# Optimization experiments

Measured on AMD Instinct MI355X. Metric: run time of the kernel, lower is better.

Reference implementation:

```python
import jax, jax.numpy as jnp
import numpy as np
import math

N_NODES = 50000
M = 200000          # number of (node, hyperedge) incidences
NE = 20000          # number of hyperedges (= hyperedge_index[1].max()+1)
NI = 8              # num_inds (inducing points)
DIN = 64            # dim_in
DV = 64             # dim_out == dim_V
NH = 4              # num_heads
DH = DV // NH


def setup_inputs() -> dict:
    key = jax.random.key(0)
    ks = jax.random.split(key, 24)
    node_idx = jax.random.randint(ks[0], (M,), 0, N_NODES, dtype=jnp.int32)
    edge_idx = jax.random.randint(ks[1], (M,), 0, NE, dtype=jnp.int32)
    # guarantee num_edges == NE (matches num_edges = max+1 in torch code)
    edge_idx = edge_idx.at[-1].set(NE - 1)
    hyperedge_index = jnp.stack([node_idx, edge_idx], axis=0)

    def lin(k, fan_in, shape):
        return jax.random.normal(k, shape, dtype=jnp.float32) / np.sqrt(fan_in)

    inp = {
        "X": jax.random.normal(ks[2], (N_NODES, DIN), dtype=jnp.float32),
        "hyperedge_index": hyperedge_index,
        "I": lin(ks[3], DV, (NI, DV)),  # xavier-ish inducing points
    }
    names = ["m0_wq", "m0_bq", "m0_wk", "m0_bk", "m0_wv", "m0_bv", "m0_wo", "m0_bo",
             "m1_wq", "m1_bq", "m1_wk", "m1_bk", "m1_wv", "m1_bv", "m1_wo", "m1_bo"]
    for i, n in enumerate(names):
        k = ks[4 + i]
        if n.endswith("b" + n[-1]) and n[3] == 'b':
            inp[n] = lin(k, DV, (DV,))
        else:
            inp[n] = lin(k, DV, (DV, DV))
    return inp


def _segment_softmax(a, seg, num_segments):
    # a: [E, NH]; segment-wise stable softmax along E grouped by seg
    amax = jax.ops.segment_max(a, seg, num_segments=num_segments)
    amax = jnp.where(jnp.isfinite(amax), amax, jnp.zeros_like(amax))
    e = jnp.exp(a - amax[seg])
    den = jax.ops.segment_sum(e, seg, num_segments=num_segments)
    return e / den[seg]


def _mab(Qin, Kin, wq, bq, wk, bk, wv, bv, wo, bo,
         q_idx, k_idx, seg, out_idx, num_segments):
    Q = Qin @ wq + bq            # [Nq, DV]
    K = Kin @ wk + bk            # [Nk, DV]
    V = Kin @ wv + bv            # [Nk, DV]
    # gather per extended edge, split into heads: [E, NH, DH]
    Qi = Q[q_idx].reshape(-1, NH, DH)
    Kj = K[k_idx].reshape(-1, NH, DH)
    Vj = V[k_idx].reshape(-1, NH, DH)
    A = (Qi * Kj).sum(-1) / math.sqrt(DV)               # [E, NH]
    A = _segment_softmax(A, seg, num_segments)           # segment softmax over LE_index
    QKV = jax.ops.segment_sum(A[..., None] * Vj, seg, num_segments=num_segments)  # [ns, NH, DH]
    O = Q[out_idx].reshape(-1, NH, DH) + QKV              # [ns, NH, DH]
    # torch: stack heads at dim0 then permute(1,2,0).reshape -> [N, DH, NH] flatten
    O = jnp.transpose(O, (0, 2, 1)).reshape(-1, DV)
    return O + jax.nn.relu(O @ wo + bo)


def reference(X, hyperedge_index, I,
              m0_wq, m0_bq, m0_wk, m0_bk, m0_wv, m0_bv, m0_wo, m0_bo,
              m1_wq, m1_bq, m1_wk, m1_bk, m1_wv, m1_bv, m1_wo, m1_bo):
    node = hyperedge_index[0]                 # [M]
    edge = hyperedge_index[1]                 # [M]
    node_t = jnp.tile(node, NI)               # [M*NI]
    edge_t = jnp.tile(edge, NI)
    inc = jnp.repeat(jnp.arange(NI, dtype=edge.dtype), M)
    ext2 = edge_t * NI + inc                  # index into I_big rows / segments for mab0

    I_big = jnp.tile(I, (NE, 1))              # [NE*NI, DV]
    # mab0: queries = inducing points (per edge), keys/values = X
    H = _mab(I_big, X,
             m0_wq, m0_bq, m0_wk, m0_bk, m0_wv, m0_bv, m0_wo, m0_bo,
             q_idx=ext2, k_idx=node_t, seg=ext2,
             out_idx=jnp.arange(NE * NI), num_segments=NE * NI)

    seg1 = jnp.tile(jnp.arange(M, dtype=edge.dtype), NI)
    # mab1: queries = X, keys/values = H; output one row per incidence
    O = _mab(X, H,
             m1_wq, m1_bq, m1_wk, m1_bk, m1_wv, m1_bv, m1_wo, m1_bo,
             q_idx=node_t, k_idx=ext2, seg=seg1,
             out_idx=node, num_segments=M)
    return O  # [M, DV]; original returns (O, None)
```

## Files before the change

kernel.cpp:

```cpp
#include <hip/hip_runtime.h>
#include <math.h>

#define NNODES 50000
#define MINC   200000
#define NEDGE  20000
#define NIND   8

#define SCALE_LOG2E 0.18033688f

typedef __attribute__((ext_vector_type(8))) short bf16x8;
typedef __attribute__((ext_vector_type(4))) float f32x4;

__device__ __forceinline__ short f2bf(float f) {
    union { float f; unsigned u; } x; x.f = f;
    unsigned r = x.u + 0x7FFF + ((x.u >> 16) & 1);
    return (short)(r >> 16);
}
__device__ __forceinline__ float bf2f(short s) {
    union { unsigned u; float f; } x; x.u = ((unsigned)(unsigned short)s) << 16;
    return x.f;
}
__device__ __forceinline__ int qperm(int c) { return ((c & 15) << 2) | (c >> 4); }
__device__ __forceinline__ int sigperm(int c) { return ((c & 3) << 4) | (c >> 2); }

__global__ void setup_hist_kernel(const float* __restrict__ I,
                                  const float* __restrict__ m0_wq, const float* __restrict__ m0_bq,
                                  const float* __restrict__ m0_wk, const float* __restrict__ m0_bk,
                                  const float* __restrict__ m0_wv, const float* __restrict__ m0_bv,
                                  const float* __restrict__ m1_wq, const float* __restrict__ m1_bq,
                                  const float* __restrict__ m0_wo, const float* __restrict__ m1_wk,
                                  const float* __restrict__ m1_wv, const float* __restrict__ m1_wo,
                                  float* __restrict__ QI, float* __restrict__ bias160,
                                  short* __restrict__ Wt0, short* __restrict__ WtO,
                                  short* __restrict__ WtK, short* __restrict__ WtV,
                                  short* __restrict__ WtF,
                                  const int* __restrict__ edge, int* __restrict__ cnt) {
    __shared__ float QIs[512];
    __shared__ float Wf[2048];
    __shared__ float bfS[32];
    int tid = threadIdx.x, bid = blockIdx.x;
    if (bid >= 6) {
        int m = (bid - 6) * 512 + tid;
        if (m < MINC) atomicAdd(&cnt[edge[m]], 1);
        return;
    }
    {
        int i = tid >> 6, c = tid & 63;
        float acc = m0_bq[c];
        for (int k = 0; k < 64; ++k) acc += I[i * 64 + k] * m0_wq[k * 64 + c];
        QIs[tid] = acc;
    }
    __syncthreads();
    if (bid == 0) {
        QI[tid] = QIs[tid];
        if (tid < 32) {
            int i = tid >> 2, h = tid & 3;
            float s = 0.f;
            for (int d = 0; d < 16; ++d)
                s += m0_bk[h * 16 + d] * QIs[i * 64 + h * 16 + d];
            bfS[tid] = s * SCALE_LOG2E;
        }
        __syncthreads();
        if (tid < 160)
            bias160[tid] = (tid < 64) ? m0_bv[tid]
                         : ((tid < 96) ? bfS[tid - 64] : m1_bq[tid - 96]);
    } else if (bid == 1) {
        for (int idx = tid; idx < 2048; idx += 512) {
            int k = idx >> 5, j = idx & 31;
            int i = j >> 2, h = j & 3;
            float s = 0.f;
            for (int d = 0; d < 16; ++d)
                s += m0_wk[k * 64 + h * 16 + d] * QIs[i * 64 + h * 16 + d];
            Wf[idx] = s * SCALE_LOG2E;
        }
        __syncthreads();
        for (int idx = tid; idx < 160 * 72; idx += 512) {
            int c = idx / 72, k = idx % 72;
            short v = 0;
            if (k < 64) {
                float f = (c < 64) ? m0_wv[k * 64 + c]
                        : (c < 96) ? Wf[k * 32 + (c - 64)]
                                   : m1_wq[k * 64 + (c - 96)];
                v = f2bf(f);
            }
            Wt0[idx] = v;
        }
    } else {
        int mat = bid - 2;
        const float* W = (mat == 0) ? m0_wo : (mat == 1) ? m1_wk : (mat == 2) ? m1_wv : m1_wo;
        short* D = (mat == 0) ? WtO : (mat == 1) ? WtK : (mat == 2) ? WtV : WtF;
        bool cperm = (mat == 0);
        for (int idx = tid; idx < 64 * 72; idx += 512) {
            int c = idx / 72, k = idx % 72;
            short v = 0;
            if (k < 64) {
                int kk = qperm(k);
                int cc = cperm ? qperm(c) : c;
                v = f2bf(W[kk * 64 + cc]);
            }
            D[idx] = v;
        }
    }
}

#define NALLOCB ((NEDGE + 255) / 256)
__global__ void gemmx_alloc_kernel(const float* __restrict__ A,
                                   const short* __restrict__ Wt, const float* __restrict__ bias,
                                   short* __restrict__ V0, _Float16* __restrict__ S0,
                                   short* __restrict__ Q1,
                                   const int* __restrict__ cnt, int2* __restrict__ rowcnt,
                                   int* __restrict__ cursor, int* __restrict__ total) {
    __shared__ short As[64 * 72];
    __shared__ short Ws[160 * 72];
    int tid = threadIdx.x;
    if (blockIdx.x < NALLOCB) {
        int e = blockIdx.x * 256 + tid;
        int lane = tid & 63;
        int c = (e < NEDGE) ? cnt[e] : 0;
        int v = c;
        #pragma unroll
        for (int off = 1; off < 64; off <<= 1) {
            int t = __shfl_up(v, off);
            if (lane >= off) v += t;
        }
        int wavesum = __shfl(v, 63);
        int base = 0;
        if (lane == 63) base = atomicAdd(total, wavesum);
        base = __shfl(base, 63);
        int excl = base + v - c;
        if (e < NEDGE) {
            rowcnt[e] = make_int2(excl, c);
            cursor[e] = excl;
        }
        return;
    }
    int row0 = (blockIdx.x - NALLOCB) * 64;
    {
        const uint4* wsrc = (const uint4*)Wt;
        uint4* wdst = (uint4*)Ws;
        for (int k = tid; k < 1440; k += 256) wdst[k] = wsrc[k];
    }
    {
        int r = tid >> 2, c0 = (tid & 3) * 16;
        int gr = row0 + r;
        float f[16];
        if (gr < NNODES) {
            const float4* src = (const float4*)(A + (size_t)gr * 64 + c0);
            #pragma unroll
            for (int j = 0; j < 4; ++j) {
                float4 t4 = src[j];
                f[4*j] = t4.x; f[4*j+1] = t4.y; f[4*j+2] = t4.z; f[4*j+3] = t4.w;
            }
        } else {
            #pragma unroll
            for (int j = 0; j < 16; ++j) f[j] = 0.f;
        }
        short tmp[16];
        #pragma unroll
        for (int j = 0; j < 16; ++j) tmp[j] = f2bf(f[j]);
        uint4* dst = (uint4*)&As[r * 72 + c0];
        dst[0] = *(const uint4*)&tmp[0];
        dst[1] = *(const uint4*)&tmp[8];
    }
    __syncthreads();
    int w = tid >> 6, l = tid & 63;
    int lr16 = l & 15, lk = (l >> 4) * 8;
    f32x4 acc[10] = {};
    #pragma unroll
    for (int ks = 0; ks < 2; ++ks) {
        bf16x8 a = *(const bf16x8*)&As[(w * 16 + lr16) * 72 + ks * 32 + lk];
        #pragma unroll
        for (int t = 0; t < 10; ++t) {
            bf16x8 b = *(const bf16x8*)&Ws[(t * 16 + lr16) * 72 + ks * 32 + lk];
            acc[t] = __builtin_amdgcn_mfma_f32_16x16x32_bf16(a, b, acc[t], 0, 0, 0);
        }
    }
    int rbase = w * 16 + (l >> 4) * 4;
    #pragma unroll
    for (int t = 0; t < 10; ++t) {
        int c = t * 16 + lr16;
        float bb = bias[c];
        #pragma unroll
        for (int r = 0; r < 4; ++r) {
            int gr = row0 + rbase + r;
            if (gr < NNODES) {
                float val = acc[t][r] + bb;
                if (c < 64) V0[(size_t)gr * 64 + c] = f2bf(val);
                else if (c < 96) S0[(size_t)gr * 32 + (c - 64)] = (_Float16)val;
                else Q1[(size_t)gr * 64 + (c - 96)] = f2bf(val);
            }
        }
    }
}

__global__ void scatter_kernel(const int* __restrict__ node, const int* __restrict__ edge,
                               int* __restrict__ cursor, int2* __restrict__ csr_nm) {
    int m = blockIdx.x * 256 + threadIdx.x;
    if (m < MINC) {
        int e = edge[m];
        int pos = atomicAdd(&cursor[e], 1);
        csr_nm[pos] = make_int2(node[m], m);
    }
}

#define CH0 32
__global__ void attn0_kernel(const short* __restrict__ V0, const _Float16* __restrict__ S0,
                             const float* __restrict__ QI,
                             const int2* __restrict__ rowcnt, const int2* __restrict__ csr_nm,
                             short* __restrict__ Opre0) {
    __shared__ float Sw[4][CH0][32];
    __shared__ float Sc[4][32];
    __shared__ float Li[4][32];
    __shared__ int   Ns[4][CH0];
    int w = threadIdx.x >> 6;
    int lane = threadIdx.x & 63;
    int e = blockIdx.x * 4 + w;
    int2 rc = rowcnt[e];
    int start = rc.x, end = rc.x + rc.y;
    int j = lane & 31;
    int pslot = lane >> 5;
    int tj = ((j & 3) << 3) | (j >> 2);
    int col2 = lane & 31;
    int hh = col2 >> 3;
    float runm = -INFINITY, lrun = 0.f;
    float accL[8] = {}, accH[8] = {};
    for (int c0 = start; c0 < end; c0 += CH0) {
        int cnt = min(CH0, end - c0);
        if (lane < CH0) {
            int idx = c0 + min(lane, cnt - 1);
            Ns[w][lane] = csr_nm[idx].x;
        }
        asm volatile("s_waitcnt lgkmcnt(0)" ::: "memory");
        __builtin_amdgcn_sched_barrier(0);
        float cm = -INFINITY;
        for (int p = pslot; p < cnt; p += 2) {
            int n = Ns[w][p];
            float s = (float)S0[(size_t)n * 32 + j];
            Sw[w][p][tj] = s;
            cm = fmaxf(cm, s);
        }
        cm = fmaxf(cm, __shfl_xor(cm, 32));
        float newm = fmaxf(runm, cm);
        float sc = exp2f(runm - newm);
        runm = newm;
        float lsum = 0.f;
        for (int p = pslot; p < cnt; p += 2) {
            float s = Sw[w][p][tj];
            float w_ = exp2f(s - newm);
            Sw[w][p][tj] = w_;
            lsum += w_;
        }
        lsum += __shfl_xor(lsum, 32);
        lrun = lrun * sc + lsum;
        if (pslot == 0) Sc[w][tj] = sc;
        asm volatile("s_waitcnt lgkmcnt(0)" ::: "memory");
        __builtin_amdgcn_sched_barrier(0);
        float4 sA = *(const float4*)&Sc[w][hh * 8];
        float4 sB = *(const float4*)&Sc[w][hh * 8 + 4];
        accL[0] *= sA.x; accH[0] *= sA.x;
        accL[1] *= sA.y; accH[1] *= sA.y;
        accL[2] *= sA.z; accH[2] *= sA.z;
        accL[3] *= sA.w; accH[3] *= sA.w;
        accL[4] *= sB.x; accH[4] *= sB.x;
        accL[5] *= sB.y; accH[5] *= sB.y;
        accL[6] *= sB.z; accH[6] *= sB.z;
        accL[7] *= sB.w; accH[7] *= sB.w;
        int npair = (cnt + 1) >> 1;
        #pragma unroll 4
        for (int k = 0; k < npair; ++k) {
            int rp = 2 * k + pslot;
            bool vld = rp < cnt;
            int rc2 = vld ? rp : (cnt - 1);
            int n = Ns[w][rc2];
            unsigned vp = *(const unsigned*)&V0[(size_t)n * 64 + col2 * 2];
            float vlo = vld ? __int_as_float(vp << 16) : 0.f;
            float vhi = vld ? __int_as_float(vp & 0xffff0000u) : 0.f;
            float4 wA = *(const float4*)&Sw[w][rc2][hh * 8];
            float4 wB = *(const float4*)&Sw[w][rc2][hh * 8 + 4];
            accL[0] += wA.x * vlo; accH[0] += wA.x * vhi;
            accL[1] += wA.y * vlo; accH[1] += wA.y * vhi;
            accL[2] += wA.z * vlo; accH[2] += wA.z * vhi;
            accL[3] += wA.w * vlo; accH[3] += wA.w * vhi;
            accL[4] += wB.x * vlo; accH[4] += wB.x * vhi;
            accL[5] += wB.y * vlo; accH[5] += wB.y * vhi;
            accL[6] += wB.z * vlo; accH[6] += wB.z * vhi;
            accL[7] += wB.w * vlo; accH[7] += wB.w * vhi;
        }
    }
    if (pslot == 0) Li[w][tj] = lrun;
    asm volatile("s_waitcnt lgkmcnt(0)" ::: "memory");
    __builtin_amdgcn_sched_barrier(0);
    #pragma unroll
    for (int i = 0; i < 8; ++i) {
        accL[i] += __shfl_xor(accL[i], 32);
        accH[i] += __shfl_xor(accH[i], 32);
    }
    float4 lA = *(const float4*)&Li[w][hh * 8];
    float4 lB = *(const float4*)&Li[w][hh * 8 + 4];
    float li[8] = {lA.x, lA.y, lA.z, lA.w, lB.x, lB.y, lB.z, lB.w};
    if (pslot == 0) {
        #pragma unroll
        for (int i = 0; i < 8; ++i) {
            float2 qi2 = *(const float2*)&QI[i * 64 + col2 * 2];
            float inv = (li[i] > 0.f) ? 1.f / li[i] : 0.f;
            float ol = qi2.x + accL[i] * inv;
            float oh = qi2.y + accH[i] * inv;
            unsigned res = ((unsigned)(unsigned short)f2bf(oh) << 16)
                         | (unsigned)(unsigned short)f2bf(ol);
            *(unsigned*)&Opre0[(size_t)(e * NIND + i) * 64 + col2 * 2] = res;
        }
    }
}

__global__ void fused_hkv_attn1_kernel(const short* __restrict__ Opre0,
                                       const short* __restrict__ WtO, const float* __restrict__ bo,
                                       const short* __restrict__ WtK, const float* __restrict__ bk,
                                       const short* __restrict__ WtV, const float* __restrict__ bv,
                                       const short* __restrict__ Q1,
                                       const int2* __restrict__ rowcnt,
                                       const int2* __restrict__ csr_nm,
                                       short* __restrict__ Opre1) {
    __shared__ short As[64 * 72];
    __shared__ short Vls[64 * 72];
    int tid = threadIdx.x;
    int row0 = blockIdx.x * 64;
    {
        int r = tid >> 2, c0 = (tid & 3) * 16;
        const uint4* src = (const uint4*)(Opre0 + (size_t)(row0 + r) * 64 + c0);
        uint4* dst = (uint4*)&As[r * 72 + c0];
        dst[0] = src[0]; dst[1] = src[1];
    }
    __syncthreads();
    int w = tid >> 6, lane = tid & 63;
    int lr16 = lane & 15, lk = (lane >> 4) * 8;
    int rbase = w * 16 + (lane >> 4) * 4;
    {
        f32x4 acc[4] = {};
        #pragma unroll
        for (int ks = 0; ks < 2; ++ks) {
            bf16x8 a = *(const bf16x8*)&As[(w * 16 + lr16) * 72 + ks * 32 + lk];
            #pragma unroll
            for (int t = 0; t < 4; ++t) {
                bf16x8 b = *(const bf16x8*)&WtO[(t * 16 + lr16) * 72 + ks * 32 + lk];
                acc[t] = __builtin_amdgcn_mfma_f32_16x16x32_bf16(a, b, acc[t], 0, 0, 0);
            }
        }
        #pragma unroll
        for (int t = 0; t < 4; ++t) {
            int c = t * 16 + lr16;
            float bb = bo[qperm(c)];
            #pragma unroll
            for (int r = 0; r < 4; ++r) {
                float res = bf2f(As[(rbase + r) * 72 + c]);
                float hv = res + fmaxf(acc[t][r] + bb, 0.f);
                As[(rbase + r) * 72 + c] = f2bf(hv);
            }
        }
    }
    {
        f32x4 ak[4] = {}, av[4] = {};
        #pragma unroll
        for (int ks = 0; ks < 2; ++ks) {
            bf16x8 a = *(const bf16x8*)&As[(w * 16 + lr16) * 72 + ks * 32 + lk];
            #pragma unroll
            for (int t = 0; t < 4; ++t) {
                bf16x8 b1 = *(const bf16x8*)&WtK[(t * 16 + lr16) * 72 + ks * 32 + lk];
                ak[t] = __builtin_amdgcn_mfma_f32_16x16x32_bf16(a, b1, ak[t], 0, 0, 0);
                bf16x8 b2 = *(const bf16x8*)&WtV[(t * 16 + lr16) * 72 + ks * 32 + lk];
                av[t] = __builtin_amdgcn_mfma_f32_16x16x32_bf16(a, b2, av[t], 0, 0, 0);
            }
        }
        #pragma unroll
        for (int t = 0; t < 4; ++t) {
            int c = t * 16 + lr16;
            float bbk = bk[c], bbv = bv[c];
            #pragma unroll
            for (int r = 0; r < 4; ++r) {
                int rr = rbase + r;
                As[rr * 72 + c]  = f2bf((ak[t][r] + bbk) * SCALE_LOG2E);
                Vls[rr * 72 + c] = f2bf(av[t][r] + bbv);
            }
        }
    }
    int sl4 = lane & 15;
    int inc = lane >> 4;
    for (int le = 0; le < 2; ++le) {
        int eloc = w * 2 + le;
        int e = blockIdx.x * 8 + eloc;
        int lr0 = eloc * 8;
        float Kf[8][4], Vf[8][4];
        #pragma unroll
        for (int i = 0; i < 8; ++i) {
            uint2 kp = *(const uint2*)&As[(lr0 + i) * 72 + sl4 * 4];
            uint2 vp = *(const uint2*)&Vls[(lr0 + i) * 72 + sl4 * 4];
            Kf[i][0] = __int_as_float(kp.x << 16);
            Kf[i][1] = __int_as_float(kp.x & 0xffff0000u);
            Kf[i][2] = __int_as_float(kp.y << 16);
            Kf[i][3] = __int_as_float(kp.y & 0xffff0000u);
            Vf[i][0] = __int_as_float(vp.x << 16);
            Vf[i][1] = __int_as_float(vp.x & 0xffff0000u);
            Vf[i][2] = __int_as_float(vp.y << 16);
            Vf[i][3] = __int_as_float(vp.y & 0xffff0000u);
        }
        #pragma unroll
        for (int i = 0; i < 8; ++i) {
            #pragma unroll
            for (int d = 0; d < 4; ++d) {
                asm volatile("" : "+v"(Kf[i][d]), "+v"(Vf[i][d]));
            }
        }
        int2 rc = rowcnt[e];
        int start = rc.x, end = rc.x + rc.y;
        #pragma unroll 4
        for (int p0 = start; p0 < end; p0 += 4) {
            int p = p0 + inc;
            bool valid = (p < end);
            int pc = valid ? p : (end - 1);
            int2 nm = csr_nm[pc];
            uint2 qp = *(const uint2*)&Q1[(size_t)nm.x * 64 + sl4 * 4];
            float qa0 = __int_as_float(qp.x << 16);
            float qa1 = __int_as_float(qp.x & 0xffff0000u);
            float qa2 = __int_as_float(qp.y << 16);
            float qa3 = __int_as_float(qp.y & 0xffff0000u);
            float a[8];
            #pragma unroll
            for (int i = 0; i < 8; ++i) {
                float t = qa0 * Kf[i][0] + qa1 * Kf[i][1] + qa2 * Kf[i][2] + qa3 * Kf[i][3];
                int tv = __builtin_amdgcn_update_dpp(0, __float_as_int(t), 0xB1, 0xf, 0xf, true);
                t += __int_as_float(tv);
                tv = __builtin_amdgcn_update_dpp(0, __float_as_int(t), 0x4E, 0xf, 0xf, true);
                t += __int_as_float(tv);
                a[i] = t;
            }
            float mx = fmaxf(fmaxf(fmaxf(a[0], a[1]), fmaxf(a[2], a[3])),
                             fmaxf(fmaxf(a[4], a[5]), fmaxf(a[6], a[7])));
            float l = 0.f, ac0 = 0.f, ac1 = 0.f, ac2 = 0.f, ac3 = 0.f;
            #pragma unroll
            for (int i = 0; i < 8; ++i) {
                float w_ = exp2f(a[i] - mx);
                l += w_;
                ac0 += w_ * Vf[i][0];
                ac1 += w_ * Vf[i][1];
                ac2 += w_ * Vf[i][2];
                ac3 += w_ * Vf[i][3];
            }
            float rl = 1.f / l;
            float o0 = qa0 + ac0 * rl;
            float o1 = qa1 + ac1 * rl;
            float o2 = qa2 + ac2 * rl;
            float o3 = qa3 + ac3 * rl;
            uint2 res;
            res.x = ((unsigned)(unsigned short)f2bf(o1) << 16) | (unsigned)(unsigned short)f2bf(o0);
            res.y = ((unsigned)(unsigned short)f2bf(o3) << 16) | (unsigned)(unsigned short)f2bf(o2);
            if (valid) *(uint2*)&Opre1[(size_t)nm.y * 64 + sl4 * 4] = res;
        }
    }
}

__global__ void gemm_out_kernel(const short* __restrict__ Av,
                                const short* __restrict__ Wt, const float* __restrict__ bias,
                                float* __restrict__ out) {
    __shared__ short As[128 * 72];
    __shared__ short Ws[64 * 72];
    int tid = threadIdx.x;
    int row0 = blockIdx.x * 128;
    {
        const uint4* wsrc = (const uint4*)Wt;
        uint4* wdst = (uint4*)Ws;
        for (int k = tid; k < 576; k += 256) wdst[k] = wsrc[k];
    }
    #pragma unroll
    for (int it = 0; it < 2; ++it) {
        int slot = tid + it * 256;
        int r = slot >> 2, c0 = (slot & 3) * 16;
        int gr = row0 + r;
        uint4 a0 = {}, a1 = {};
        if (gr < MINC) {
            const uint4* src = (const uint4*)(Av + (size_t)gr * 64 + c0);
            a0 = src[0]; a1 = src[1];
        }
        uint4* dst = (uint4*)&As[r * 72 + c0];
        dst[0] = a0; dst[1] = a1;
    }
    __syncthreads();
    int w = tid >> 6, l = tid & 63;
    int lr16 = l & 15, lk = (l >> 4) * 8;
    f32x4 acc[2][4] = {};
    #pragma unroll
    for (int ks = 0; ks < 2; ++ks) {
        bf16x8 a0 = *(const bf16x8*)&As[(w * 16 + lr16) * 72 + ks * 32 + lk];
        bf16x8 a1 = *(const bf16x8*)&As[(64 + w * 16 + lr16) * 72 + ks * 32 + lk];
        #pragma unroll
        for (int t = 0; t < 4; ++t) {
            bf16x8 b = *(const bf16x8*)&Ws[(t * 16 + lr16) * 72 + ks * 32 + lk];
            acc[0][t] = __builtin_amdgcn_mfma_f32_16x16x32_bf16(a0, b, acc[0][t], 0, 0, 0);
            acc[1][t] = __builtin_amdgcn_mfma_f32_16x16x32_bf16(a1, b, acc[1][t], 0, 0, 0);
        }
    }
    int rbase = w * 16 + (l >> 4) * 4;
    #pragma unroll
    for (int rt = 0; rt < 2; ++rt) {
        #pragma unroll
        for (int t = 0; t < 4; ++t) {
            int c = t * 16 + lr16;
            float bb = bias[c];
            int sc = sigperm(c);
            #pragma unroll
            for (int r = 0; r < 4; ++r) {
                int gr = row0 + rt * 64 + rbase + r;
                if (gr < MINC) {
                    float val = acc[rt][t][r] + bb;
                    float res = bf2f(As[(rt * 64 + rbase + r) * 72 + sc]);
                    __builtin_nontemporal_store(res + fmaxf(val, 0.f),
                                                &out[(size_t)gr * 64 + c]);
                }
            }
        }
    }
}

extern "C" void kernel_launch(void* const* d_in, const int* in_sizes, int n_in,
                              void* d_out, int out_size, void* d_ws, size_t ws_size,
                              hipStream_t stream) {
    const float* X    = (const float*)d_in[0];
    const int*   hei  = (const int*)d_in[1];
    const float* I    = (const float*)d_in[2];
    const float* m0_wq = (const float*)d_in[3];
    const float* m0_bq = (const float*)d_in[4];
    const float* m0_wk = (const float*)d_in[5];
    const float* m0_bk = (const float*)d_in[6];
    const float* m0_wv = (const float*)d_in[7];
    const float* m0_bv = (const float*)d_in[8];
    const float* m0_wo = (const float*)d_in[9];
    const float* m0_bo = (const float*)d_in[10];
    const float* m1_wq = (const float*)d_in[11];
    const float* m1_bq = (const float*)d_in[12];
    const float* m1_wk = (const float*)d_in[13];
    const float* m1_bk = (const float*)d_in[14];
    const float* m1_wv = (const float*)d_in[15];
    const float* m1_bv = (const float*)d_in[16];
    const float* m1_wo = (const float*)d_in[17];
    const float* m1_bo = (const float*)d_in[18];

    const int* node = hei;
    const int* edge = hei + MINC;
    float* out = (float*)d_out;

    char* B = (char*)d_ws;
    short* Opre0 = (short*)B;
    short* V0    = (short*)(B + 20480000);
    _Float16* S0 = (_Float16*)(B + 26880000);
    short* Opre1 = (short*)(B + 33280000);
    short* Q1    = (short*)(B + 74240000);
    float* QI    = (float*)(B + 80640000);
    float* bias160 = QI + 512;
    short* PK    = (short*)(bias160 + 160);
    short* Wt0   = PK;
    short* WtO   = PK + 11520;
    short* WtK   = WtO + 4608;
    short* WtV   = WtK + 4608;
    short* WtF   = WtV + 4608;
    int*   ib       = (int*)(((size_t)(WtF + 4608) + 7) & ~(size_t)7);
    int2*  rowcnt   = (int2*)ib;
    int*   cnt      = (int*)(rowcnt + NEDGE);
    int*   total    = cnt + NEDGE;
    int*   cursor   = total + 1;
    int2*  csr_nm   = (int2*)(((size_t)(cursor + NEDGE) + 7) & ~(size_t)7);

    hipMemsetAsync(cnt, 0, (NEDGE + 1) * sizeof(int), stream);
    setup_hist_kernel<<<6 + (MINC + 511) / 512, 512, 0, stream>>>(
        I, m0_wq, m0_bq, m0_wk, m0_bk, m0_wv, m0_bv,
        m1_wq, m1_bq, m0_wo, m1_wk, m1_wv, m1_wo,
        QI, bias160, Wt0, WtO, WtK, WtV, WtF, edge, cnt);
    gemmx_alloc_kernel<<<NALLOCB + (NNODES + 63) / 64, 256, 0, stream>>>(
        X, Wt0, bias160, V0, S0, Q1, cnt, rowcnt, cursor, total);
    scatter_kernel<<<(MINC + 255) / 256, 256, 0, stream>>>(node, edge, cursor, csr_nm);

    attn0_kernel<<<NEDGE / 4, 256, 0, stream>>>(V0, S0, QI, rowcnt, csr_nm, Opre0);

    fused_hkv_attn1_kernel<<<NEDGE / 8, 256, 0, stream>>>(
        Opre0, WtO, m0_bo, WtK, m1_bk, WtV, m1_bv, Q1, rowcnt, csr_nm, Opre1);
    gemm_out_kernel<<<(MINC + 127) / 128, 256, 0, stream>>>(Opre1, WtF, m1_bo, out);
}
```

Baseline: 146.9 us.

## Fuse first-MAB attention into the H/K/V + second attention kernel

The separate attn0 kernel is merged into the fused H-projection/attn1 kernel. Each wave now computes the inducing-point attention for two hyperedges and writes the bf16 result straight into its own LDS rows, instead of round-tripping the Opre0 buffer through global memory. This removes one kernel launch and the global write and re-read of that intermediate, and compacts the workspace layout. In exchange, each wave processes its two edges serially, the grid has half as many waves for the attention phase, and per-block LDS grows, which may lower occupancy.

After: 149.0 us. Within noise of the previous version (+1.4%).

```diff
diff --git a/kernel.cpp b/kernel.cpp
--- a/kernel.cpp
+++ b/kernel.cpp
@@ -204,134 +204,125 @@
 }
 
 #define CH0 32
-__global__ void attn0_kernel(const short* __restrict__ V0, const _Float16* __restrict__ S0,
-                             const float* __restrict__ QI,
-                             const int2* __restrict__ rowcnt, const int2* __restrict__ csr_nm,
-                             short* __restrict__ Opre0) {
+__global__ void mega_mab1_kernel(const short* __restrict__ V0, const _Float16* __restrict__ S0,
+                                 const float* __restrict__ QI,
+                                 const short* __restrict__ WtO, const float* __restrict__ bo,
+                                 const short* __restrict__ WtK, const float* __restrict__ bk,
+                                 const short* __restrict__ WtV, const float* __restrict__ bv,
+                                 const short* __restrict__ Q1,
+                                 const int2* __restrict__ rowcnt,
+                                 const int2* __restrict__ csr_nm,
+                                 short* __restrict__ Opre1) {
+    __shared__ short As[64 * 72];
+    __shared__ short Vls[64 * 72];
     __shared__ float Sw[4][CH0][32];
     __shared__ float Sc[4][32];
     __shared__ float Li[4][32];
     __shared__ int   Ns[4][CH0];
-    int w = threadIdx.x >> 6;
-    int lane = threadIdx.x & 63;
-    int e = blockIdx.x * 4 + w;
-    int2 rc = rowcnt[e];
-    int start = rc.x, end = rc.x + rc.y;
+    int tid = threadIdx.x;
+    int w = tid >> 6, lane = tid & 63;
+
     int j = lane & 31;
     int pslot = lane >> 5;
     int tj = ((j & 3) << 3) | (j >> 2);
     int col2 = lane & 31;
     int hh = col2 >> 3;
-    float runm = -INFINITY, lrun = 0.f;
-    float accL[8] = {}, accH[8] = {};
-    for (int c0 = start; c0 < end; c0 += CH0) {
-        int cnt = min(CH0, end - c0);
-        if (lane < CH0) {
-            int idx = c0 + min(lane, cnt - 1);
-            Ns[w][lane] = csr_nm[idx].x;
-        }
+    for (int le = 0; le < 2; ++le) {
+        int e = blockIdx.x * 8 + w * 2 + le;
+        int2 rc = rowcnt[e];
+        int start = rc.x, end = rc.x + rc.y;
+        float runm = -INFINITY, lrun = 0.f;
+        float accL[8] = {}, accH[8] = {};
+        for (int c0 = start; c0 < end; c0 += CH0) {
+            int cnt = min(CH0, end - c0);
+            if (lane < CH0) {
+                int idx = c0 + min(lane, cnt - 1);
+                Ns[w][lane] = csr_nm[idx].x;
+            }
+            asm volatile("s_waitcnt lgkmcnt(0)" ::: "memory");
+            __builtin_amdgcn_sched_barrier(0);
+            float cm = -INFINITY;
+            for (int p = pslot; p < cnt; p += 2) {
+                int n = Ns[w][p];
+                float s = (float)S0[(size_t)n * 32 + j];
+                Sw[w][p][tj] = s;
+                cm = fmaxf(cm, s);
+            }
+            cm = fmaxf(cm, __shfl_xor(cm, 32));
+            float newm = fmaxf(runm, cm);
+            float sc = exp2f(runm - newm);
+            runm = newm;
+            float lsum = 0.f;
+            for (int p = pslot; p < cnt; p += 2) {
+                float s = Sw[w][p][tj];
+                float w_ = exp2f(s - newm);
+                Sw[w][p][tj] = w_;
+                lsum += w_;
+            }
+            lsum += __shfl_xor(lsum, 32);
+            lrun = lrun * sc + lsum;
+            if (pslot == 0) Sc[w][tj] = sc;
+            asm volatile("s_waitcnt lgkmcnt(0)" ::: "memory");
+            __builtin_amdgcn_sched_barrier(0);
+            float4 sA = *(const float4*)&Sc[w][hh * 8];
+            float4 sB = *(const float4*)&Sc[w][hh * 8 + 4];
+            accL[0] *= sA.x; accH[0] *= sA.x;
+            accL[1] *= sA.y; accH[1] *= sA.y;
+            accL[2] *= sA.z; accH[2] *= sA.z;
+            accL[3] *= sA.w; accH[3] *= sA.w;
+            accL[4] *= sB.x; accH[4] *= sB.x;
+            accL[5] *= sB.y; accH[5] *= sB.y;
+            accL[6] *= sB.z; accH[6] *= sB.z;
+            accL[7] *= sB.w; accH[7] *= sB.w;
+            int npair = (cnt + 1) >> 1;
+            #pragma unroll 4
+            for (int k = 0; k < npair; ++k) {
+                int rp = 2 * k + pslot;
+                bool vld = rp < cnt;
+                int rc2 = vld ? rp : (cnt - 1);
+                int n = Ns[w][rc2];
+                unsigned vp = *(const unsigned*)&V0[(size_t)n * 64 + col2 * 2];
+                float vlo = vld ? __int_as_float(vp << 16) : 0.f;
+                float vhi = vld ? __int_as_float(vp & 0xffff0000u) : 0.f;
+                float4 wA = *(const float4*)&Sw[w][rc2][hh * 8];
+                float4 wB = *(const float4*)&Sw[w][rc2][hh * 8 + 4];
+                accL[0] += wA.x * vlo; accH[0] += wA.x * vhi;
+                accL[1] += wA.y * vlo; accH[1] += wA.y * vhi;
+                accL[2] += wA.z * vlo; accH[2] += wA.z * vhi;
+                accL[3] += wA.w * vlo; accH[3] += wA.w * vhi;
+                accL[4] += wB.x * vlo; accH[4] += wB.x * vhi;
+                accL[5] += wB.y * vlo; accH[5] += wB.y * vhi;
+                accL[6] += wB.z * vlo; accH[6] += wB.z * vhi;
+                accL[7] += wB.w * vlo; accH[7] += wB.w * vhi;
+            }
+        }
+        if (pslot == 0) Li[w][tj] = lrun;
         asm volatile("s_waitcnt lgkmcnt(0)" ::: "memory");
         __builtin_amdgcn_sched_barrier(0);
-        float cm = -INFINITY;
-        for (int p = pslot; p < cnt; p += 2) {
-            int n = Ns[w][p];
-            float s = (float)S0[(size_t)n * 32 + j];
-            Sw[w][p][tj] = s;
-            cm = fmaxf(cm, s);
-        }
-        cm = fmaxf(cm, __shfl_xor(cm, 32));
-        float newm = fmaxf(runm, cm);
-        float sc = exp2f(runm - newm);
-        runm = newm;
-        float lsum = 0.f;
-        for (int p = pslot; p < cnt; p += 2) {
-            float s = Sw[w][p][tj];
-            float w_ = exp2f(s - newm);
-            Sw[w][p][tj] = w_;
-            lsum += w_;
-        }
-        lsum += __shfl_xor(lsum, 32);
-        lrun = lrun * sc + lsum;
-        if (pslot == 0) Sc[w][tj] = sc;
-        asm volatile("s_waitcnt lgkmcnt(0)" ::: "memory");
-        __builtin_amdgcn_sched_barrier(0);
-        float4 sA = *(const float4*)&Sc[w][hh * 8];
-        float4 sB = *(const float4*)&Sc[w][hh * 8 + 4];
-        accL[0] *= sA.x; accH[0] *= sA.x;
-        accL[1] *= sA.y; accH[1] *= sA.y;
-        accL[2] *= sA.z; accH[2] *= sA.z;
-        accL[3] *= sA.w; accH[3] *= sA.w;
-        accL[4] *= sB.x; accH[4] *= sB.x;
-        accL[5] *= sB.y; accH[5] *= sB.y;
-        accL[6] *= sB.z; accH[6] *= sB.z;
-        accL[7] *= sB.w; accH[7] *= sB.w;
-        int npair = (cnt + 1) >> 1;
-        #pragma unroll 4
-        for (int k = 0; k < npair; ++k) {
-            int rp = 2 * k + pslot;
-            bool vld = rp < cnt;
-            int rc2 = vld ? rp : (cnt - 1);
-            int n = Ns[w][rc2];
-            unsigned vp = *(const unsigned*)&V0[(size_t)n * 64 + col2 * 2];
-            float vlo = vld ? __int_as_float(vp << 16) : 0.f;
-            float vhi = vld ? __int_as_float(vp & 0xffff0000u) : 0.f;
-            float4 wA = *(const float4*)&Sw[w][rc2][hh * 8];
-            float4 wB = *(const float4*)&Sw[w][rc2][hh * 8 + 4];
-            accL[0] += wA.x * vlo; accH[0] += wA.x * vhi;
-            accL[1] += wA.y * vlo; accH[1] += wA.y * vhi;
-            accL[2] += wA.z * vlo; accH[2] += wA.z * vhi;
-            accL[3] += wA.w * vlo; accH[3] += wA.w * vhi;
-            accL[4] += wB.x * vlo; accH[4] += wB.x * vhi;
-            accL[5] += wB.y * vlo; accH[5] += wB.y * vhi;
-            accL[6] += wB.z * vlo; accH[6] += wB.z * vhi;
-            accL[7] += wB.w * vlo; accH[7] += wB.w * vhi;
-        }
-    }
-    if (pslot == 0) Li[w][tj] = lrun;
+        #pragma unroll
+        for (int i = 0; i < 8; ++i) {
+            accL[i] += __shfl_xor(accL[i], 32);
+            accH[i] += __shfl_xor(accH[i], 32);
+        }
+        float4 lA = *(const float4*)&Li[w][hh * 8];
+        float4 lB = *(const float4*)&Li[w][hh * 8 + 4];
+        float li[8] = {lA.x, lA.y, lA.z, lA.w, lB.x, lB.y, lB.z, lB.w};
+        if (pslot == 0) {
+            #pragma unroll
+            for (int i = 0; i < 8; ++i) {
+                float2 qi2 = *(const float2*)&QI[i * 64 + col2 * 2];
+                float inv = (li[i] > 0.f) ? 1.f / li[i] : 0.f;
+                float ol = qi2.x + accL[i] * inv;
+                float oh = qi2.y + accH[i] * inv;
+                unsigned res = ((unsigned)(unsigned short)f2bf(oh) << 16)
+                             | (unsigned)(unsigned short)f2bf(ol);
+                *(unsigned*)&As[(w * 16 + le * 8 + i) * 72 + col2 * 2] = res;
+            }
+        }
+    }
     asm volatile("s_waitcnt lgkmcnt(0)" ::: "memory");
     __builtin_amdgcn_sched_barrier(0);
-    #pragma unroll
-    for (int i = 0; i < 8; ++i) {
-        accL[i] += __shfl_xor(accL[i], 32);
-        accH[i] += __shfl_xor(accH[i], 32);
-    }
-    float4 lA = *(const float4*)&Li[w][hh * 8];
-    float4 lB = *(const float4*)&Li[w][hh * 8 + 4];
-    float li[8] = {lA.x, lA.y, lA.z, lA.w, lB.x, lB.y, lB.z, lB.w};
-    if (pslot == 0) {
-        #pragma unroll
-        for (int i = 0; i < 8; ++i) {
-            float2 qi2 = *(const float2*)&QI[i * 64 + col2 * 2];
-            float inv = (li[i] > 0.f) ? 1.f / li[i] : 0.f;
-            float ol = qi2.x + accL[i] * inv;
-            float oh = qi2.y + accH[i] * inv;
-            unsigned res = ((unsigned)(unsigned short)f2bf(oh) << 16)
-                         | (unsigned)(unsigned short)f2bf(ol);
-            *(unsigned*)&Opre0[(size_t)(e * NIND + i) * 64 + col2 * 2] = res;
-        }
-    }
-}
-
-__global__ void fused_hkv_attn1_kernel(const short* __restrict__ Opre0,
-                                       const short* __restrict__ WtO, const float* __restrict__ bo,
-                                       const short* __restrict__ WtK, const float* __restrict__ bk,
-                                       const short* __restrict__ WtV, const float* __restrict__ bv,
-                                       const short* __restrict__ Q1,
-                                       const int2* __restrict__ rowcnt,
-                                       const int2* __restrict__ csr_nm,
-                                       short* __restrict__ Opre1) {
-    __shared__ short As[64 * 72];
-    __shared__ short Vls[64 * 72];
-    int tid = threadIdx.x;
-    int row0 = blockIdx.x * 64;
-    {
-        int r = tid >> 2, c0 = (tid & 3) * 16;
-        const uint4* src = (const uint4*)(Opre0 + (size_t)(row0 + r) * 64 + c0);
-        uint4* dst = (uint4*)&As[r * 72 + c0];
-        dst[0] = src[0]; dst[1] = src[1];
-    }
-    __syncthreads();
-    int w = tid >> 6, lane = tid & 63;
+
     int lr16 = lane & 15, lk = (lane >> 4) * 8;
     int rbase = w * 16 + (lane >> 4) * 4;
     {
@@ -382,6 +373,9 @@
             }
         }
     }
+    asm volatile("s_waitcnt lgkmcnt(0)" ::: "memory");
+    __builtin_amdgcn_sched_barrier(0);
+
     int sl4 = lane & 15;
     int inc = lane >> 4;
     for (int le = 0; le < 2; ++le) {
@@ -547,12 +541,11 @@
     float* out = (float*)d_out;
 
     char* B = (char*)d_ws;
-    short* Opre0 = (short*)B;
-    short* V0    = (short*)(B + 20480000);
-    _Float16* S0 = (_Float16*)(B + 26880000);
-    short* Opre1 = (short*)(B + 33280000);
-    short* Q1    = (short*)(B + 74240000);
-    float* QI    = (float*)(B + 80640000);
+    short* Opre1 = (short*)B;
+    short* V0    = (short*)(B + 26000000);
+    _Float16* S0 = (_Float16*)(B + 33000000);
+    short* Q1    = (short*)(B + 37000000);
+    float* QI    = (float*)(B + 44000000);
     float* bias160 = QI + 512;
     short* PK    = (short*)(bias160 + 160);
     short* Wt0   = PK;
@@ -576,9 +569,8 @@
         X, Wt0, bias160, V0, S0, Q1, cnt, rowcnt, cursor, total);
     scatter_kernel<<<(MINC + 255) / 256, 256, 0, stream>>>(node, edge, cursor, csr_nm);
 
-    attn0_kernel<<<NEDGE / 4, 256, 0, stream>>>(V0, S0, QI, rowcnt, csr_nm, Opre0);
-
-    fused_hkv_attn1_kernel<<<NEDGE / 8, 256, 0, stream>>>(
-        Opre0, WtO, m0_bo, WtK, m1_bk, WtV, m1_bv, Q1, rowcnt, csr_nm, Opre1);
+    mega_mab1_kernel<<<NEDGE / 8, 256, 0, stream>>>(
+        V0, S0, QI, WtO, m0_bo, WtK, m1_bk, WtV, m1_bv, Q1, rowcnt, csr_nm, Opre1);
+
     gemm_out_kernel<<<(MINC + 127) / 128, 256, 0, stream>>>(Opre1, WtF, m1_bo, out);
 }
```
